# Performance work log

Hardware: AMD Instinct MI355X
Metric: run time of the kernel (lower is better)

## Reference

```python
import jax, jax.numpy as jnp
import numpy as np
import math

D_MODEL = 2048
N_HEADS = 16
D_K = D_MODEL // N_HEADS
B = 4
S = 2048


def setup_inputs() -> dict:
    key = jax.random.key(0)
    ks = jax.random.split(key, 12)
    sd = 1.0 / math.sqrt(D_MODEL)
    inp = {
        "query": jax.random.normal(ks[0], (B, S, D_MODEL), dtype=jnp.float32),
        "key": jax.random.normal(ks[1], (B, S, D_MODEL), dtype=jnp.float32),
        "value": jax.random.normal(ks[2], (B, S, D_MODEL), dtype=jnp.float32),
        # causal mask: 1 where attendable, 0 where masked (mask == 0 -> -1e9)
        "mask": jnp.tril(jnp.ones((1, 1, S, S), dtype=jnp.int32)),
        "W_q": jax.random.uniform(ks[3], (D_MODEL, D_MODEL), jnp.float32, -sd, sd),
        "b_q": jnp.zeros((D_MODEL,), jnp.float32),
        "W_k": jax.random.uniform(ks[4], (D_MODEL, D_MODEL), jnp.float32, -sd, sd),
        "b_k": jnp.zeros((D_MODEL,), jnp.float32),
        "W_v": jax.random.uniform(ks[5], (D_MODEL, D_MODEL), jnp.float32, -sd, sd),
        "b_v": jnp.zeros((D_MODEL,), jnp.float32),
        "W_o": jax.random.uniform(ks[6], (D_MODEL, D_MODEL), jnp.float32, -sd, sd),
        "b_o": jnp.zeros((D_MODEL,), jnp.float32),
    }
    return inp


def reference(query, key, value, mask, W_q, b_q, W_k, b_k, W_v, b_v, W_o, b_o):
    scale = math.sqrt(D_K)
    # QKV projections + split heads: [B, S, D] -> [B, H, S, d_k]
    def split_heads(x):
        return x.reshape(B, -1, N_HEADS, D_K).transpose(0, 2, 1, 3)

    Q = split_heads(query @ W_q.T + b_q)
    K = split_heads(key @ W_k.T + b_k)
    V = split_heads(value @ W_v.T + b_v)

    # scores: [B, H, Sq, Sk]
    scores = jnp.einsum("bhqd,bhkd->bhqk", Q, K) / scale
    scores = jnp.where(mask == 0, jnp.float32(-1e9), scores)
    attn = jax.nn.softmax(scores, axis=-1)
    # context: [B, H, Sq, d_k] -> [B, Sq, D]
    ctx = jnp.einsum("bhqk,bhkd->bhqd", attn, V)
    ctx = ctx.transpose(0, 2, 1, 3).reshape(B, S, D_MODEL)
    return ctx @ W_o.T + b_o
```

## Files before the change

kernel.cpp:

```cpp
#include <hip/hip_runtime.h>
#include <stdint.h>

#define D_MODEL 2048
#define S_LEN 2048
#define BATCH 4
#define NHEADS 16
#define DK 128
#define M_TOK (BATCH * S_LEN)

typedef __attribute__((ext_vector_type(8))) short bf16x8;
typedef __attribute__((ext_vector_type(4))) float f32x4;

__device__ __forceinline__ short f2bf(float f) {
  unsigned u = __float_as_uint(f);
  u = (u + 0x7FFF + ((u >> 16) & 1)) >> 16;
  return (short)u;
}
__device__ __forceinline__ short f2bf_fast(float f) {
  return (short)((__float_as_uint(f) + 0x8000u) >> 16);
}

__device__ __forceinline__ void gl2lds16(const void* g, void* l) {
  __builtin_amdgcn_global_load_lds(
      (const __attribute__((address_space(1))) unsigned int*)g,
      (__attribute__((address_space(3))) unsigned int*)l, 16, 0, 0);
}

#define ASM_BAR() asm volatile("s_barrier" ::: "memory")
#define VMCNT0() asm volatile("s_waitcnt vmcnt(0)" ::: "memory")

__global__ __launch_bounds__(256) void cvt3_kernel(const float* __restrict__ a0,
                                                   const float* __restrict__ a1,
                                                   const float* __restrict__ a2,
                                                   short* o0, short* o1,
                                                   short* o2, int n8) {
  const float* in = (blockIdx.y == 0) ? a0 : (blockIdx.y == 1) ? a1 : a2;
  short* out = (blockIdx.y == 0) ? o0 : (blockIdx.y == 1) ? o1 : o2;
  int i = blockIdx.x * blockDim.x + threadIdx.x;
  const int stride = gridDim.x * blockDim.x;
  for (; i < n8; i += stride) {
    const float4* p = (const float4*)(in + (size_t)i * 8);
    float4 a = p[0], b = p[1];
    bf16x8 o;
    o[0] = f2bf(a.x); o[1] = f2bf(a.y); o[2] = f2bf(a.z); o[3] = f2bf(a.w);
    o[4] = f2bf(b.x); o[5] = f2bf(b.y); o[6] = f2bf(b.z); o[7] = f2bf(b.w);
    *(bf16x8*)(out + (size_t)i * 8) = o;
  }
}

__global__ __launch_bounds__(256) void cvt4_kernel(const float* __restrict__ a0,
                                                   const float* __restrict__ a1,
                                                   const float* __restrict__ a2,
                                                   const float* __restrict__ a3,
                                                   short* o0, short* o1,
                                                   short* o2, short* o3,
                                                   int n8) {
  const float* in = (blockIdx.y == 0)   ? a0
                    : (blockIdx.y == 1) ? a1
                    : (blockIdx.y == 2) ? a2
                                        : a3;
  short* out = (blockIdx.y == 0)   ? o0
               : (blockIdx.y == 1) ? o1
               : (blockIdx.y == 2) ? o2
                                   : o3;
  int i = blockIdx.x * blockDim.x + threadIdx.x;
  const int stride = gridDim.x * blockDim.x;
  for (; i < n8; i += stride) {
    const float4* p = (const float4*)(in + (size_t)i * 8);
    float4 a = p[0], b = p[1];
    bf16x8 o;
    o[0] = f2bf(a.x); o[1] = f2bf(a.y); o[2] = f2bf(a.z); o[3] = f2bf(a.w);
    o[4] = f2bf(b.x); o[5] = f2bf(b.y); o[6] = f2bf(b.z); o[7] = f2bf(b.w);
    *(bf16x8*)(out + (size_t)i * 8) = o;
  }
}

template <int EPI>
__global__ __launch_bounds__(512, 2) void gemm256(const short* __restrict__ A,
                                                  const short* __restrict__ B,
                                                  const float* __restrict__ bias,
                                                  void* __restrict__ Cout,
                                                  float escale) {
  __shared__ short As[2][256 * 64];
  __shared__ short Bs[2][256 * 64];
  const int t = threadIdx.x, lane = t & 63, w = t >> 6;
  const int c = lane & 15, g = lane >> 4;
  const int wr = w >> 2, wc = w & 3;

  const int cpx = (int)gridDim.x >> 3;
  const int swz = ((int)blockIdx.x & 7) * cpx + ((int)blockIdx.x >> 3);
  const int by = swz >> 3, bx = swz & 7;
  const int row0 = by * 256, col0 = bx * 256;
  const int K = D_MODEL;
  const int NT = K / 64;

  const int srow = t >> 3;
  const int sseg = t & 7;
  const int skk = 8 * (sseg ^ (srow & 7));

  const short* Abase = A + (size_t)(row0 + srow) * K;
  const short* Bbase = B + (size_t)(col0 + srow) * K;

#define SWEEPA(p, R, kt)                                              \
  gl2lds16(Abase + (size_t)(R) * 64 * K + (kt) * 64 + skk,            \
           &As[p][(R) * 4096 + t * 8])
#define SWEEPB(p, R, kt)                                              \
  gl2lds16(Bbase + (size_t)(R) * 64 * K + (kt) * 64 + skk,            \
           &Bs[p][(R) * 4096 + t * 8])
#define STAGE_TILE(q, kt1)                                            \
  {                                                                   \
    SWEEPA(q, 0, kt1); SWEEPA(q, 1, kt1);                             \
    SWEEPA(q, 2, kt1); SWEEPA(q, 3, kt1);                             \
    SWEEPB(q, 0, kt1); SWEEPB(q, 1, kt1);                             \
    SWEEPB(q, 2, kt1); SWEEPB(q, 3, kt1);                             \
  }

  f32x4 acc[8][4] = {};

  STAGE_TILE(0, 0);

  for (int kt = 0; kt < NT; ++kt) {
    const int p = kt & 1, q = p ^ 1;
    VMCNT0();
    ASM_BAR();
    if (kt + 1 < NT) STAGE_TILE(q, kt + 1);

    const char* abase = (const char*)As[p];
    const char* bbase = (const char*)Bs[p];
#pragma unroll
    for (int ks = 0; ks < 2; ++ks) {
      const int kb = (ks * 64 + g * 16) ^ ((c & 7) << 4);
      bf16x8 bfr[4];
#pragma unroll
      for (int ni = 0; ni < 4; ++ni)
        bfr[ni] = *(const bf16x8*)(bbase + (wc * 64 + ni * 16 + c) * 128 + kb);
#pragma unroll
      for (int mg = 0; mg < 2; ++mg) {
        bf16x8 afr[4];
#pragma unroll
        for (int mi = 0; mi < 4; ++mi)
          afr[mi] = *(const bf16x8*)(abase +
                                     (wr * 128 + mg * 64 + mi * 16 + c) * 128 +
                                     kb);
        __builtin_amdgcn_s_setprio(1);
#pragma unroll
        for (int mi = 0; mi < 4; ++mi)
#pragma unroll
          for (int ni = 0; ni < 4; ++ni) {
            if (EPI == 2)
              acc[mg * 4 + mi][ni] = __builtin_amdgcn_mfma_f32_16x16x32_bf16(
                  afr[mi], bfr[ni], acc[mg * 4 + mi][ni], 0, 0, 0);
            else
              acc[mg * 4 + mi][ni] = __builtin_amdgcn_mfma_f32_16x16x32_bf16(
                  bfr[ni], afr[mi], acc[mg * 4 + mi][ni], 0, 0, 0);
          }
        __builtin_amdgcn_s_setprio(0);
      }
    }
  }

  if (EPI == 2) {
#pragma unroll
    for (int ni = 0; ni < 4; ++ni) {
      const int col = col0 + wc * 64 + ni * 16 + c;
      const float bv = bias[col];
#pragma unroll
      for (int m = 0; m < 8; ++m) {
        const int rbase =
            row0 + wr * 128 + (m >> 2) * 64 + (m & 3) * 16 + g * 4;
        const int h = col >> 7, dk = col & 127;
        const int b = rbase >> 11, s0 = rbase & 2047;
        ushort4 pk;
        pk.x = (unsigned short)f2bf(acc[m][ni][0] + bv);
        pk.y = (unsigned short)f2bf(acc[m][ni][1] + bv);
        pk.z = (unsigned short)f2bf(acc[m][ni][2] + bv);
        pk.w = (unsigned short)f2bf(acc[m][ni][3] + bv);
        *(ushort4*)&((short*)Cout)[(((size_t)b * NHEADS + h) * DK + dk) *
                                       S_LEN + s0] = pk;
      }
    }
  } else {
#pragma unroll
    for (int ni = 0; ni < 4; ++ni) {
      const int col = col0 + wc * 64 + ni * 16 + g * 4;
      const float4 bv4 = *(const float4*)&bias[col];
#pragma unroll
      for (int m = 0; m < 8; ++m) {
        const int s = row0 + wr * 128 + (m >> 2) * 64 + (m & 3) * 16 + c;
        if (EPI == 0) {
          const int h = col >> 7, dk = col & 127;
          const int b = s >> 11, ss = s & 2047;
          ushort4 pk;
          pk.x = (unsigned short)f2bf((acc[m][ni][0] + bv4.x) * escale);
          pk.y = (unsigned short)f2bf((acc[m][ni][1] + bv4.y) * escale);
          pk.z = (unsigned short)f2bf((acc[m][ni][2] + bv4.z) * escale);
          pk.w = (unsigned short)f2bf((acc[m][ni][3] + bv4.w) * escale);
          *(ushort4*)&((short*)Cout)[(((size_t)b * NHEADS + h) * S_LEN + ss) *
                                         DK + dk] = pk;
        } else {
          float4 v;
          v.x = acc[m][ni][0] + bv4.x;
          v.y = acc[m][ni][1] + bv4.y;
          v.z = acc[m][ni][2] + bv4.z;
          v.w = acc[m][ni][3] + bv4.w;
          *(float4*)&((float*)Cout)[(size_t)s * D_MODEL + col] = v;
        }
      }
    }
  }
#undef SWEEPA
#undef SWEEPB
#undef STAGE_TILE
}

__global__ __launch_bounds__(256, 2) void attn_kernel(
    const short* __restrict__ Qp, const short* __restrict__ Kp,
    const short* __restrict__ Vt, short* __restrict__ ctx) {
  const int t = threadIdx.x, lane = t & 63, w = t >> 6;
  const int c = lane & 15, g = lane >> 4;

  const int fid = blockIdx.x;
  const int x = fid & 7, u = fid >> 3;
  const int bh = ((u & 7) << 3) | x;
  const int qt = 15 - (u >> 3);
  const int b = bh >> 4, h = bh & 15;

  __shared__ short Kl[2][64 * 128];
  __shared__ short Vl[2][128 * 64];
  __shared__ short Pl[4][32][64];

  const short* Kbase = Kp + (size_t)bh * S_LEN * DK;
  const short* Vbase = Vt + (size_t)bh * DK * S_LEN;

  const int qbase = qt * 128 + w * 32;
  const short* Qg = Qp + ((size_t)bh * S_LEN + qbase + c) * DK;
  bf16x8 aq[2][4];
#pragma unroll
  for (int mi = 0; mi < 2; ++mi)
#pragma unroll
    for (int kc = 0; kc < 4; ++kc)
      aq[mi][kc] = *(const bf16x8*)(Qg + mi * 16 * DK + kc * 32 + g * 8);

  float mprev[2][4], lsum[2][4];
  f32x4 accO[2][8] = {};
#pragma unroll
  for (int mi = 0; mi < 2; ++mi)
#pragma unroll
    for (int r = 0; r < 4; ++r) {
      mprev[mi][r] = -3.0e38f;
      lsum[mi][r] = 0.f;
    }

  const int nt = 2 * qt + 2;
  const int jmax = (qbase + 31) >> 6;

  auto stage = [&](int buf, int j) {
    const short* Kg = Kbase + (size_t)j * 64 * DK;
#pragma unroll
    for (int ii = 0; ii < 4; ++ii) {
      int s = t + 256 * ii;
      int row = s >> 4, cs = s & 15;
      gl2lds16(Kg + row * DK + (cs ^ (row & 7)) * 8, &Kl[buf][s * 8]);
    }
    const short* Vg = Vbase + j * 64;
#pragma unroll
    for (int ii = 0; ii < 4; ++ii) {
      int s = t + 256 * ii;
      int row = s >> 3, cs = s & 7;
      gl2lds16(Vg + (size_t)row * S_LEN + (cs ^ (row & 7)) * 8,
               &Vl[buf][s * 8]);
    }
  };

  stage(0, 0);
  __syncthreads();
  int cur = 0;

  for (int j = 0; j < nt; ++j) {
    if (j + 1 < nt) stage(cur ^ 1, j + 1);

    if (j <= jmax) {
      f32x4 sa[2][4];
#pragma unroll
      for (int mi = 0; mi < 2; ++mi)
#pragma unroll
        for (int nf = 0; nf < 4; ++nf) sa[mi][nf] = (f32x4){0.f, 0.f, 0.f, 0.f};
      __builtin_amdgcn_s_setprio(1);
#pragma unroll
      for (int nf = 0; nf < 4; ++nf) {
#pragma unroll
        for (int kc = 0; kc < 4; ++kc) {
          const int row = nf * 16 + c;
          const int seg = kc * 4 + g;
          bf16x8 bk = *(const bf16x8*)((const char*)&Kl[cur][0] + row * 256 +
                                       ((seg ^ (row & 7)) << 4));
#pragma unroll
          for (int mi = 0; mi < 2; ++mi)
            sa[mi][nf] = __builtin_amdgcn_mfma_f32_16x16x32_bf16(
                aq[mi][kc], bk, sa[mi][nf], 0, 0, 0);
        }
      }
      __builtin_amdgcn_s_setprio(0);

#pragma unroll
      for (int mi = 0; mi < 2; ++mi) {
        if (j * 64 + 63 > qbase + mi * 16) {
#pragma unroll
          for (int r = 0; r < 4; ++r) {
            const int qglob = qbase + mi * 16 + g * 4 + r;
#pragma unroll
            for (int nf = 0; nf < 4; ++nf)
              if ((j * 64 + nf * 16 + c) > qglob) sa[mi][nf][r] = -3.0e38f;
          }
        }
      }

      float lmax[2][4];
      bool need = false;
#pragma unroll
      for (int mi = 0; mi < 2; ++mi)
#pragma unroll
        for (int r = 0; r < 4; ++r) {
          const float m0 = fmaxf(fmaxf(sa[mi][0][r], sa[mi][1][r]),
                                 fmaxf(sa[mi][2][r], sa[mi][3][r]));
          lmax[mi][r] = m0;
          need = need || (m0 > mprev[mi][r] + 5.101f);
        }
      if (__any((int)need)) {
#pragma unroll
        for (int mi = 0; mi < 2; ++mi)
#pragma unroll
          for (int r = 0; r < 4; ++r) {
            float m0 = lmax[mi][r];
            m0 = fmaxf(m0, __shfl_xor(m0, 1));
            m0 = fmaxf(m0, __shfl_xor(m0, 2));
            m0 = fmaxf(m0, __shfl_xor(m0, 4));
            m0 = fmaxf(m0, __shfl_xor(m0, 8));
            const float nm = fmaxf(mprev[mi][r], m0);
            const float corr = exp2f(mprev[mi][r] - nm);
            lsum[mi][r] *= corr;
#pragma unroll
            for (int no = 0; no < 8; ++no) accO[mi][no][r] *= corr;
            mprev[mi][r] = nm;
          }
      }

#pragma unroll
      for (int mi = 0; mi < 2; ++mi)
#pragma unroll
        for (int r = 0; r < 4; ++r) {
          const float nm = mprev[mi][r];
          const int prow = mi * 16 + g * 4 + r;
          float rs = 0.f;
#pragma unroll
          for (int nf = 0; nf < 4; ++nf) {
            const float pp = exp2f(sa[mi][nf][r] - nm);
            rs += pp;
            const int col = nf * 16 + c;
            *(short*)((char*)&Pl[w][0][0] + prow * 128 +
                      (((col >> 3) ^ (prow & 7)) << 4) + (col & 7) * 2) =
                f2bf_fast(pp);
          }
          lsum[mi][r] += rs;
        }

      bf16x8 ap[2][2];
#pragma unroll
      for (int mi = 0; mi < 2; ++mi)
#pragma unroll
        for (int kc = 0; kc < 2; ++kc) {
          const int prow = mi * 16 + c;
          const int kseg = kc * 4 + g;
          ap[mi][kc] = *(const bf16x8*)((const char*)&Pl[w][0][0] +
                                        prow * 128 +
                                        ((kseg ^ (prow & 7)) << 4));
        }
      __builtin_amdgcn_s_setprio(1);
#pragma unroll
      for (int no = 0; no < 8; ++no) {
#pragma unroll
        for (int kc = 0; kc < 2; ++kc) {
          const int row = no * 16 + c;
          const int seg = kc * 4 + g;
          bf16x8 bv = *(const bf16x8*)((const char*)&Vl[cur][0] + row * 128 +
                                       ((seg ^ (row & 7)) << 4));
#pragma unroll
          for (int mi = 0; mi < 2; ++mi)
            accO[mi][no] = __builtin_amdgcn_mfma_f32_16x16x32_bf16(
                ap[mi][kc], bv, accO[mi][no], 0, 0, 0);
        }
      }
      __builtin_amdgcn_s_setprio(0);
    }

    __syncthreads();
    cur ^= 1;
  }

#pragma unroll
  for (int mi = 0; mi < 2; ++mi) {
    const int qrow = qbase + mi * 16 + g * 4;
#pragma unroll
    for (int r = 0; r < 4; ++r) {
      float ls = lsum[mi][r];
      ls += __shfl_xor(ls, 1);
      ls += __shfl_xor(ls, 2);
      ls += __shfl_xor(ls, 4);
      ls += __shfl_xor(ls, 8);
      const float inv = 1.f / ls;
#pragma unroll
      for (int no = 0; no < 8; ++no) {
        ctx[((size_t)b * S_LEN + qrow + r) * D_MODEL + h * DK + no * 16 + c] =
            f2bf_fast(accO[mi][no][r] * inv);
      }
    }
  }
}

extern "C" void kernel_launch(void* const* d_in, const int* in_sizes, int n_in,
                              void* d_out, int out_size, void* d_ws,
                              size_t ws_size, hipStream_t stream) {
  const float* query = (const float*)d_in[0];
  const float* key = (const float*)d_in[1];
  const float* value = (const float*)d_in[2];
  const float* W_q = (const float*)d_in[4];
  const float* b_q = (const float*)d_in[5];
  const float* W_k = (const float*)d_in[6];
  const float* b_k = (const float*)d_in[7];
  const float* W_v = (const float*)d_in[8];
  const float* b_v = (const float*)d_in[9];
  const float* W_o = (const float*)d_in[10];
  const float* b_o = (const float*)d_in[11];
  float* out = (float*)d_out;

  char* p = (char*)d_ws;
  const size_t WSZ = (size_t)D_MODEL * D_MODEL * 2;
  const size_t XSZ = (size_t)M_TOK * D_MODEL * 2;
  short* wq = (short*)p; p += WSZ;
  short* wk = (short*)p; p += WSZ;
  short* wv = (short*)p; p += WSZ;
  short* wo = (short*)p; p += WSZ;
  short* xq = (short*)p; p += XSZ;
  short* xk = (short*)p; p += XSZ;
  short* xv = (short*)p; p += XSZ;
  short* Qp = (short*)p; p += XSZ;
  short* Kp = (short*)p; p += XSZ;
  short* Vt = (short*)p; p += XSZ;

  const int nX8 = (M_TOK * D_MODEL) / 8;
  const int nW8 = (D_MODEL * D_MODEL) / 8;
  cvt3_kernel<<<dim3(1024, 3), 256, 0, stream>>>(query, key, value, xq, xk, xv,
                                                 nX8);
  cvt4_kernel<<<dim3(512, 4), 256, 0, stream>>>(W_q, W_k, W_v, W_o, wq, wk, wv,
                                                wo, nW8);

  const float qscale = 0.12753101829629947f;
  const int ngemm = (M_TOK / 256) * (D_MODEL / 256);

  gemm256<0><<<ngemm, 512, 0, stream>>>(xq, wq, b_q, Qp, qscale);
  gemm256<0><<<ngemm, 512, 0, stream>>>(xk, wk, b_k, Kp, 1.0f);
  gemm256<2><<<ngemm, 512, 0, stream>>>(xv, wv, b_v, Vt, 1.0f);

  attn_kernel<<<dim3(16 * BATCH * NHEADS), 256, 0, stream>>>(Qp, Kp, Vt, xq);

  gemm256<1><<<256, 512, 0, stream>>>(xq, wo, b_o, out, 1.0f);
}
```

Before: 496.2 us.

## Fuse fp32-to-bf16 activation conversion into QKV projection GEMM loads

Removes the separate conversion kernel for query/key/value and has the projection GEMMs read fp32 activations straight into registers. They are packed to bf16 with v_cvt_pk_bf16_f32 and written to LDS after the MFMA work of the current tile. This saves a full read/write pass over three 64 MB activation tensors. In exchange the GEMM A loads double in bytes, go through registers instead of direct global-to-LDS copies, and use extra VGPRs. Conversion also changes from round-to-nearest-even to the hardware packed convert.

```diff
diff --git a/kernel.cpp b/kernel.cpp
--- a/kernel.cpp
+++ b/kernel.cpp
@@ -27,26 +27,7 @@
 }
 
 #define ASM_BAR() asm volatile("s_barrier" ::: "memory")
-#define VMCNT0() asm volatile("s_waitcnt vmcnt(0)" ::: "memory")
-
-__global__ __launch_bounds__(256) void cvt3_kernel(const float* __restrict__ a0,
-                                                   const float* __restrict__ a1,
-                                                   const float* __restrict__ a2,
-                                                   short* o0, short* o1,
-                                                   short* o2, int n8) {
-  const float* in = (blockIdx.y == 0) ? a0 : (blockIdx.y == 1) ? a1 : a2;
-  short* out = (blockIdx.y == 0) ? o0 : (blockIdx.y == 1) ? o1 : o2;
-  int i = blockIdx.x * blockDim.x + threadIdx.x;
-  const int stride = gridDim.x * blockDim.x;
-  for (; i < n8; i += stride) {
-    const float4* p = (const float4*)(in + (size_t)i * 8);
-    float4 a = p[0], b = p[1];
-    bf16x8 o;
-    o[0] = f2bf(a.x); o[1] = f2bf(a.y); o[2] = f2bf(a.z); o[3] = f2bf(a.w);
-    o[4] = f2bf(b.x); o[5] = f2bf(b.y); o[6] = f2bf(b.z); o[7] = f2bf(b.w);
-    *(bf16x8*)(out + (size_t)i * 8) = o;
-  }
-}
+#define WAIT_ALL() asm volatile("s_waitcnt vmcnt(0) lgkmcnt(0)" ::: "memory")
 
 __global__ __launch_bounds__(256) void cvt4_kernel(const float* __restrict__ a0,
                                                    const float* __restrict__ a1,
@@ -75,8 +56,8 @@
   }
 }
 
-template <int EPI>
-__global__ __launch_bounds__(512, 2) void gemm256(const short* __restrict__ A,
+template <int EPI, int AF32>
+__global__ __launch_bounds__(512, 2) void gemm256(const void* __restrict__ Ain,
                                                   const short* __restrict__ B,
                                                   const float* __restrict__ bias,
                                                   void* __restrict__ Cout,
@@ -98,32 +79,68 @@
   const int sseg = t & 7;
   const int skk = 8 * (sseg ^ (srow & 7));
 
-  const short* Abase = A + (size_t)(row0 + srow) * K;
+  const short* Abase = (const short*)Ain + (size_t)(row0 + srow) * K;
+  const float* Afbase = (const float*)Ain + (size_t)(row0 + srow) * K;
   const short* Bbase = B + (size_t)(col0 + srow) * K;
 
-#define SWEEPA(p, R, kt)                                              \
-  gl2lds16(Abase + (size_t)(R) * 64 * K + (kt) * 64 + skk,            \
-           &As[p][(R) * 4096 + t * 8])
-#define SWEEPB(p, R, kt)                                              \
-  gl2lds16(Bbase + (size_t)(R) * 64 * K + (kt) * 64 + skk,            \
-           &Bs[p][(R) * 4096 + t * 8])
-#define STAGE_TILE(q, kt1)                                            \
-  {                                                                   \
-    SWEEPA(q, 0, kt1); SWEEPA(q, 1, kt1);                             \
-    SWEEPA(q, 2, kt1); SWEEPA(q, 3, kt1);                             \
-    SWEEPB(q, 0, kt1); SWEEPB(q, 1, kt1);                             \
-    SWEEPB(q, 2, kt1); SWEEPB(q, 3, kt1);                             \
-  }
+  float4 a4[8];
+
+  auto stage_tile = [&](int q, int kt1) {
+    if (AF32) {
+#pragma unroll
+      for (int R = 0; R < 4; ++R) {
+        const float4* s =
+            (const float4*)(Afbase + (size_t)R * 64 * K + kt1 * 64 + skk);
+        a4[R * 2] = s[0];
+        a4[R * 2 + 1] = s[1];
+      }
+    } else {
+#pragma unroll
+      for (int R = 0; R < 4; ++R)
+        gl2lds16(Abase + (size_t)R * 64 * K + kt1 * 64 + skk,
+                 &As[q][R * 4096 + t * 8]);
+    }
+#pragma unroll
+    for (int R = 0; R < 4; ++R)
+      gl2lds16(Bbase + (size_t)R * 64 * K + kt1 * 64 + skk,
+               &Bs[q][R * 4096 + t * 8]);
+  };
+
+  auto flushA = [&](int q) {
+    if (AF32) {
+#pragma unroll
+      for (int R = 0; R < 4; ++R) {
+        unsigned w0, w1, w2, w3;
+        asm("v_cvt_pk_bf16_f32 %0, %1, %2"
+            : "=v"(w0)
+            : "v"(a4[R * 2].x), "v"(a4[R * 2].y));
+        asm("v_cvt_pk_bf16_f32 %0, %1, %2"
+            : "=v"(w1)
+            : "v"(a4[R * 2].z), "v"(a4[R * 2].w));
+        asm("v_cvt_pk_bf16_f32 %0, %1, %2"
+            : "=v"(w2)
+            : "v"(a4[R * 2 + 1].x), "v"(a4[R * 2 + 1].y));
+        asm("v_cvt_pk_bf16_f32 %0, %1, %2"
+            : "=v"(w3)
+            : "v"(a4[R * 2 + 1].z), "v"(a4[R * 2 + 1].w));
+        uint4 pk4;
+        pk4.x = w0; pk4.y = w1; pk4.z = w2; pk4.w = w3;
+        *(uint4*)&As[q][R * 4096 + t * 8] = pk4;
+      }
+    }
+  };
 
   f32x4 acc[8][4] = {};
 
-  STAGE_TILE(0, 0);
+  stage_tile(0, 0);
+  flushA(0);
+  WAIT_ALL();
+  ASM_BAR();
 
   for (int kt = 0; kt < NT; ++kt) {
     const int p = kt & 1, q = p ^ 1;
-    VMCNT0();
-    ASM_BAR();
-    if (kt + 1 < NT) STAGE_TILE(q, kt + 1);
+    const bool more = (kt + 1 < NT);
+    if (more) stage_tile(q, kt + 1);
 
     const char* abase = (const char*)As[p];
     const char* bbase = (const char*)Bs[p];
@@ -157,6 +174,10 @@
         __builtin_amdgcn_s_setprio(0);
       }
     }
+
+    if (more) flushA(q);
+    WAIT_ALL();
+    ASM_BAR();
   }
 
   if (EPI == 2) {
@@ -208,9 +229,6 @@
       }
     }
   }
-#undef SWEEPA
-#undef SWEEPB
-#undef STAGE_TILE
 }
 
 __global__ __launch_bounds__(256, 2) void attn_kernel(
@@ -440,28 +458,23 @@
   short* wk = (short*)p; p += WSZ;
   short* wv = (short*)p; p += WSZ;
   short* wo = (short*)p; p += WSZ;
-  short* xq = (short*)p; p += XSZ;
-  short* xk = (short*)p; p += XSZ;
-  short* xv = (short*)p; p += XSZ;
+  short* ctxb = (short*)p; p += XSZ;
   short* Qp = (short*)p; p += XSZ;
   short* Kp = (short*)p; p += XSZ;
   short* Vt = (short*)p; p += XSZ;
 
-  const int nX8 = (M_TOK * D_MODEL) / 8;
   const int nW8 = (D_MODEL * D_MODEL) / 8;
-  cvt3_kernel<<<dim3(1024, 3), 256, 0, stream>>>(query, key, value, xq, xk, xv,
-                                                 nX8);
   cvt4_kernel<<<dim3(512, 4), 256, 0, stream>>>(W_q, W_k, W_v, W_o, wq, wk, wv,
                                                 wo, nW8);
 
   const float qscale = 0.12753101829629947f;
   const int ngemm = (M_TOK / 256) * (D_MODEL / 256);
 
-  gemm256<0><<<ngemm, 512, 0, stream>>>(xq, wq, b_q, Qp, qscale);
-  gemm256<0><<<ngemm, 512, 0, stream>>>(xk, wk, b_k, Kp, 1.0f);
-  gemm256<2><<<ngemm, 512, 0, stream>>>(xv, wv, b_v, Vt, 1.0f);
-
-  attn_kernel<<<dim3(16 * BATCH * NHEADS), 256, 0, stream>>>(Qp, Kp, Vt, xq);
-
-  gemm256<1><<<256, 512, 0, stream>>>(xq, wo, b_o, out, 1.0f);
-}
+  gemm256<0, 1><<<ngemm, 512, 0, stream>>>(query, wq, b_q, Qp, qscale);
+  gemm256<0, 1><<<ngemm, 512, 0, stream>>>(key, wk, b_k, Kp, 1.0f);
+  gemm256<2, 1><<<ngemm, 512, 0, stream>>>(value, wv, b_v, Vt, 1.0f);
+
+  attn_kernel<<<dim3(16 * BATCH * NHEADS), 256, 0, stream>>>(Qp, Kp, Vt, ctxb);
+
+  gemm256<1, 0><<<256, 512, 0, stream>>>(ctxb, wo, b_o, out, 1.0f);
+}
```

After: 491.8 us, median of 3. About the same (-0.9%).

## Split GEMM K-step into four quadrant phases with interleaved async LDS loads

Applied to the files above, without the earlier changes.

Restructures the projection GEMM main loop so each K-tile is computed as four 128x128 quadrants. Each quadrant's LDS fragment reads are followed by issuing two of the next tile's global-to-LDS loads, with fine-grained vmcnt waits and barriers, instead of one full wait plus barrier per tile. The warp-to-output mapping changes so that each wave covers a 64x32 piece of every quadrant, which lets quadrant loads land while other quadrants compute. This adds more barriers per tile and carries a risk of wait-count ordering mistakes.

```diff
diff --git a/kernel.cpp b/kernel.cpp
--- a/kernel.cpp
+++ b/kernel.cpp
@@ -27,7 +27,8 @@
 }
 
 #define ASM_BAR() asm volatile("s_barrier" ::: "memory")
-#define VMCNT0() asm volatile("s_waitcnt vmcnt(0)" ::: "memory")
+#define LGKM0() asm volatile("s_waitcnt lgkmcnt(0)" ::: "memory")
+#define VMC(N) asm volatile("s_waitcnt vmcnt(" #N ")" ::: "memory")
 
 __global__ __launch_bounds__(256) void cvt3_kernel(const float* __restrict__ a0,
                                                    const float* __restrict__ a1,
@@ -101,116 +102,154 @@
   const short* Abase = A + (size_t)(row0 + srow) * K;
   const short* Bbase = B + (size_t)(col0 + srow) * K;
 
-#define SWEEPA(p, R, kt)                                              \
-  gl2lds16(Abase + (size_t)(R) * 64 * K + (kt) * 64 + skk,            \
-           &As[p][(R) * 4096 + t * 8])
-#define SWEEPB(p, R, kt)                                              \
-  gl2lds16(Bbase + (size_t)(R) * 64 * K + (kt) * 64 + skk,            \
-           &Bs[p][(R) * 4096 + t * 8])
-#define STAGE_TILE(q, kt1)                                            \
-  {                                                                   \
-    SWEEPA(q, 0, kt1); SWEEPA(q, 1, kt1);                             \
-    SWEEPA(q, 2, kt1); SWEEPA(q, 3, kt1);                             \
-    SWEEPB(q, 0, kt1); SWEEPB(q, 1, kt1);                             \
-    SWEEPB(q, 2, kt1); SWEEPB(q, 3, kt1);                             \
-  }
-
-  f32x4 acc[8][4] = {};
-
-  STAGE_TILE(0, 0);
+#define SWEEPA(pp, R, kt1)                                            \
+  gl2lds16(Abase + (size_t)(R) * 64 * K + (kt1) * 64 + skk,           \
+           &As[pp][(R) * 4096 + t * 8])
+#define SWEEPB(pp, R, kt1)                                            \
+  gl2lds16(Bbase + (size_t)(R) * 64 * K + (kt1) * 64 + skk,           \
+           &Bs[pp][(R) * 4096 + t * 8])
+
+  f32x4 acc[4][4][2] = {};
+
+#define RD(QR, QC)                                                         \
+  _Pragma("unroll") for (int ks = 0; ks < 2; ++ks) {                       \
+    const int kb = (ks * 64 + g * 16) ^ ((c & 7) << 4);                    \
+    _Pragma("unroll") for (int mi = 0; mi < 4; ++mi)                       \
+      afr[ks][mi] = *(const bf16x8*)(                                      \
+          abase + ((QR) * 128 + wr * 64 + mi * 16 + c) * 128 + kb);        \
+    _Pragma("unroll") for (int ni = 0; ni < 2; ++ni)                       \
+      bfr[ks][ni] = *(const bf16x8*)(                                      \
+          bbase + ((QC) * 128 + wc * 32 + ni * 16 + c) * 128 + kb);        \
+  }
+
+#define MM(QI)                                                             \
+  __builtin_amdgcn_s_setprio(1);                                           \
+  _Pragma("unroll") for (int ks = 0; ks < 2; ++ks)                         \
+    _Pragma("unroll") for (int mi = 0; mi < 4; ++mi)                       \
+      _Pragma("unroll") for (int ni = 0; ni < 2; ++ni) {                   \
+        if (EPI == 2)                                                      \
+          acc[QI][mi][ni] = __builtin_amdgcn_mfma_f32_16x16x32_bf16(       \
+              afr[ks][mi], bfr[ks][ni], acc[QI][mi][ni], 0, 0, 0);         \
+        else                                                               \
+          acc[QI][mi][ni] = __builtin_amdgcn_mfma_f32_16x16x32_bf16(       \
+              bfr[ks][ni], afr[ks][mi], acc[QI][mi][ni], 0, 0, 0);         \
+      }                                                                    \
+  __builtin_amdgcn_s_setprio(0);                                           \
+  __builtin_amdgcn_sched_barrier(0);
+
+  SWEEPA(0, 0, 0); SWEEPA(0, 1, 0);
+  SWEEPB(0, 0, 0); SWEEPB(0, 1, 0);
+  SWEEPB(0, 2, 0); SWEEPB(0, 3, 0);
+  SWEEPA(0, 2, 0); SWEEPA(0, 3, 0);
+  VMC(4);
+  ASM_BAR();
 
   for (int kt = 0; kt < NT; ++kt) {
     const int p = kt & 1, q = p ^ 1;
-    VMCNT0();
-    ASM_BAR();
-    if (kt + 1 < NT) STAGE_TILE(q, kt + 1);
-
+    const bool more = (kt + 1 < NT);
     const char* abase = (const char*)As[p];
     const char* bbase = (const char*)Bs[p];
-#pragma unroll
-    for (int ks = 0; ks < 2; ++ks) {
-      const int kb = (ks * 64 + g * 16) ^ ((c & 7) << 4);
-      bf16x8 bfr[4];
-#pragma unroll
-      for (int ni = 0; ni < 4; ++ni)
-        bfr[ni] = *(const bf16x8*)(bbase + (wc * 64 + ni * 16 + c) * 128 + kb);
-#pragma unroll
-      for (int mg = 0; mg < 2; ++mg) {
-        bf16x8 afr[4];
-#pragma unroll
-        for (int mi = 0; mi < 4; ++mi)
-          afr[mi] = *(const bf16x8*)(abase +
-                                     (wr * 128 + mg * 64 + mi * 16 + c) * 128 +
-                                     kb);
-        __builtin_amdgcn_s_setprio(1);
-#pragma unroll
-        for (int mi = 0; mi < 4; ++mi)
-#pragma unroll
-          for (int ni = 0; ni < 4; ++ni) {
-            if (EPI == 2)
-              acc[mg * 4 + mi][ni] = __builtin_amdgcn_mfma_f32_16x16x32_bf16(
-                  afr[mi], bfr[ni], acc[mg * 4 + mi][ni], 0, 0, 0);
-            else
-              acc[mg * 4 + mi][ni] = __builtin_amdgcn_mfma_f32_16x16x32_bf16(
-                  bfr[ni], afr[mi], acc[mg * 4 + mi][ni], 0, 0, 0);
+    {
+      bf16x8 afr[2][4], bfr[2][2];
+      RD(0, 0);
+      if (more) { SWEEPA(q, 0, kt + 1); SWEEPA(q, 1, kt + 1); }
+      ASM_BAR(); LGKM0();
+      MM(0);
+      if (more) { VMC(4); } else { VMC(2); }
+      ASM_BAR();
+    }
+    {
+      bf16x8 afr[2][4], bfr[2][2];
+      RD(0, 1);
+      if (more) { SWEEPB(q, 0, kt + 1); SWEEPB(q, 1, kt + 1); }
+      ASM_BAR(); LGKM0();
+      MM(1);
+      if (more) { VMC(4); } else { VMC(0); }
+      ASM_BAR();
+    }
+    {
+      bf16x8 afr[2][4], bfr[2][2];
+      RD(1, 1);
+      if (more) { SWEEPB(q, 2, kt + 1); SWEEPB(q, 3, kt + 1); }
+      ASM_BAR(); LGKM0();
+      MM(3);
+      ASM_BAR();
+    }
+    {
+      bf16x8 afr[2][4], bfr[2][2];
+      RD(1, 0);
+      if (more) { SWEEPA(q, 2, kt + 1); SWEEPA(q, 3, kt + 1); }
+      ASM_BAR(); LGKM0();
+      MM(2);
+      if (more) { VMC(4); }
+      ASM_BAR();
+    }
+  }
+
+  if (EPI == 2) {
+#pragma unroll
+    for (int qr2 = 0; qr2 < 2; ++qr2)
+#pragma unroll
+      for (int qc2 = 0; qc2 < 2; ++qc2) {
+        const int qi = qr2 * 2 + qc2;
+#pragma unroll
+        for (int ni = 0; ni < 2; ++ni) {
+          const int col = col0 + qc2 * 128 + wc * 32 + ni * 16 + c;
+          const float bv = bias[col];
+          const int h = col >> 7, dk = col & 127;
+#pragma unroll
+          for (int mi = 0; mi < 4; ++mi) {
+            const int rbase = row0 + qr2 * 128 + wr * 64 + mi * 16 + g * 4;
+            const int b = rbase >> 11, s0 = rbase & 2047;
+            ushort4 pk;
+            pk.x = (unsigned short)f2bf(acc[qi][mi][ni][0] + bv);
+            pk.y = (unsigned short)f2bf(acc[qi][mi][ni][1] + bv);
+            pk.z = (unsigned short)f2bf(acc[qi][mi][ni][2] + bv);
+            pk.w = (unsigned short)f2bf(acc[qi][mi][ni][3] + bv);
+            *(ushort4*)&((short*)Cout)[(((size_t)b * NHEADS + h) * DK + dk) *
+                                           S_LEN + s0] = pk;
           }
-        __builtin_amdgcn_s_setprio(0);
-      }
-    }
-  }
-
-  if (EPI == 2) {
-#pragma unroll
-    for (int ni = 0; ni < 4; ++ni) {
-      const int col = col0 + wc * 64 + ni * 16 + c;
-      const float bv = bias[col];
-#pragma unroll
-      for (int m = 0; m < 8; ++m) {
-        const int rbase =
-            row0 + wr * 128 + (m >> 2) * 64 + (m & 3) * 16 + g * 4;
-        const int h = col >> 7, dk = col & 127;
-        const int b = rbase >> 11, s0 = rbase & 2047;
-        ushort4 pk;
-        pk.x = (unsigned short)f2bf(acc[m][ni][0] + bv);
-        pk.y = (unsigned short)f2bf(acc[m][ni][1] + bv);
-        pk.z = (unsigned short)f2bf(acc[m][ni][2] + bv);
-        pk.w = (unsigned short)f2bf(acc[m][ni][3] + bv);
-        *(ushort4*)&((short*)Cout)[(((size_t)b * NHEADS + h) * DK + dk) *
-                                       S_LEN + s0] = pk;
-      }
-    }
+        }
+      }
   } else {
 #pragma unroll
-    for (int ni = 0; ni < 4; ++ni) {
-      const int col = col0 + wc * 64 + ni * 16 + g * 4;
-      const float4 bv4 = *(const float4*)&bias[col];
-#pragma unroll
-      for (int m = 0; m < 8; ++m) {
-        const int s = row0 + wr * 128 + (m >> 2) * 64 + (m & 3) * 16 + c;
-        if (EPI == 0) {
-          const int h = col >> 7, dk = col & 127;
-          const int b = s >> 11, ss = s & 2047;
-          ushort4 pk;
-          pk.x = (unsigned short)f2bf((acc[m][ni][0] + bv4.x) * escale);
-          pk.y = (unsigned short)f2bf((acc[m][ni][1] + bv4.y) * escale);
-          pk.z = (unsigned short)f2bf((acc[m][ni][2] + bv4.z) * escale);
-          pk.w = (unsigned short)f2bf((acc[m][ni][3] + bv4.w) * escale);
-          *(ushort4*)&((short*)Cout)[(((size_t)b * NHEADS + h) * S_LEN + ss) *
-                                         DK + dk] = pk;
-        } else {
-          float4 v;
-          v.x = acc[m][ni][0] + bv4.x;
-          v.y = acc[m][ni][1] + bv4.y;
-          v.z = acc[m][ni][2] + bv4.z;
-          v.w = acc[m][ni][3] + bv4.w;
-          *(float4*)&((float*)Cout)[(size_t)s * D_MODEL + col] = v;
-        }
-      }
-    }
+    for (int qr2 = 0; qr2 < 2; ++qr2)
+#pragma unroll
+      for (int qc2 = 0; qc2 < 2; ++qc2) {
+        const int qi = qr2 * 2 + qc2;
+#pragma unroll
+        for (int ni = 0; ni < 2; ++ni) {
+          const int col = col0 + qc2 * 128 + wc * 32 + ni * 16 + g * 4;
+          const float4 bv4 = *(const float4*)&bias[col];
+#pragma unroll
+          for (int mi = 0; mi < 4; ++mi) {
+            const int s = row0 + qr2 * 128 + wr * 64 + mi * 16 + c;
+            if (EPI == 0) {
+              const int h = col >> 7, dk = col & 127;
+              const int b = s >> 11, ss = s & 2047;
+              ushort4 pk;
+              pk.x = (unsigned short)f2bf((acc[qi][mi][ni][0] + bv4.x) * escale);
+              pk.y = (unsigned short)f2bf((acc[qi][mi][ni][1] + bv4.y) * escale);
+              pk.z = (unsigned short)f2bf((acc[qi][mi][ni][2] + bv4.z) * escale);
+              pk.w = (unsigned short)f2bf((acc[qi][mi][ni][3] + bv4.w) * escale);
+              *(ushort4*)&((short*)Cout)[(((size_t)b * NHEADS + h) * S_LEN +
+                                          ss) * DK + dk] = pk;
+            } else {
+              float4 v;
+              v.x = acc[qi][mi][ni][0] + bv4.x;
+              v.y = acc[qi][mi][ni][1] + bv4.y;
+              v.z = acc[qi][mi][ni][2] + bv4.z;
+              v.w = acc[qi][mi][ni][3] + bv4.w;
+              *(float4*)&((float*)Cout)[(size_t)s * D_MODEL + col] = v;
+            }
+          }
+        }
+      }
   }
 #undef SWEEPA
 #undef SWEEPB
-#undef STAGE_TILE
+#undef RD
+#undef MM
 }
 
 __global__ __launch_bounds__(256, 2) void attn_kernel(
```

Measured after the change: 543.6 us. 9.6% more time.
